# Kernel tuning notes

Hardware: AMD Instinct MI355X
Metric: run time of the kernel (lower is better)

The kernel has to match this reference:

```python
import jax, jax.numpy as jnp
import numpy as np

B, S, D, H = 4, 2048, 1024, 16
DK = D // H  # 64


def setup_inputs() -> dict:
    key = jax.random.key(0)
    ks = jax.random.split(key, 9)
    x = jax.random.normal(ks[0], (B, S, D), dtype=jnp.float32)
    # causal mask, broadcast over batch and heads
    attn_mask = jnp.tril(jnp.ones((S, S), dtype=jnp.int32))[None, None]
    scale = 0.02
    Wq = jax.random.normal(ks[1], (D, D), dtype=jnp.float32) * scale
    Wk = jax.random.normal(ks[2], (D, D), dtype=jnp.float32) * scale
    Wv = jax.random.normal(ks[3], (D, D), dtype=jnp.float32) * scale
    Wo = jax.random.normal(ks[4], (D, D), dtype=jnp.float32) * scale
    bq = jax.random.normal(ks[5], (D,), dtype=jnp.float32) * scale
    bk = jax.random.normal(ks[6], (D,), dtype=jnp.float32) * scale
    bv = jax.random.normal(ks[7], (D,), dtype=jnp.float32) * scale
    bo = jax.random.normal(ks[8], (D,), dtype=jnp.float32) * scale
    return {"x": x, "attn_mask": attn_mask, "Wq": Wq, "bq": bq, "Wk": Wk,
            "bk": bk, "Wv": Wv, "bv": bv, "Wo": Wo, "bo": bo}


def reference(x, attn_mask, Wq, bq, Wk, bk, Wv, bv, Wo, bo):
    b, s, d = x.shape
    # projections -> [b, h, s, dk]
    def proj(W, bias):
        return (x @ W + bias).reshape(b, s, H, DK).transpose(0, 2, 1, 3)
    q = proj(Wq, bq)
    k = proj(Wk, bk)
    v = proj(Wv, bv)
    # scores [b, h, s, s]
    scores = jnp.einsum('bhqd,bhkd->bhqk', q, k) / jnp.sqrt(jnp.float32(DK))
    scores = jnp.where(attn_mask == 0, jnp.float32(-1e9), scores)
    probs = jax.nn.softmax(scores, axis=-1)  # dropout_rate=0 -> identity
    attn_out = jnp.einsum('bhqk,bhkd->bhqd', probs, v)
    # combine heads -> [b, s, d], then output projection
    attn_out = attn_out.transpose(0, 2, 1, 3).reshape(b, s, d)
    return attn_out @ Wo + bo
```

## Files before the change

kernel.cpp:

```cpp
#include <hip/hip_runtime.h>
#include <hip/hip_bf16.h>
#include <stdint.h>

#define S_LEN 2048
#define DMODEL 1024
#define NH 16
#define DK 64
#define BATCH 4
#define KDIM 1024
#define SCQ 0.18033688f

using bf16 = __hip_bfloat16;
using bf162 = __hip_bfloat162;

typedef __bf16 v_bf16x8 __attribute__((ext_vector_type(8)));
typedef short v_s16x4 __attribute__((ext_vector_type(4)));
typedef float v_f32x4 __attribute__((ext_vector_type(4)));

union PackB4 { v_s16x4 v; bf162 h[2]; };

__device__ __forceinline__ void gll16(const void* g, void* l) {
    __builtin_amdgcn_global_load_lds(
        (__attribute__((address_space(1))) unsigned int*)g,
        (__attribute__((address_space(3))) unsigned int*)l, 16, 0, 0);
}

struct alignas(8) BF4 { bf16 a, b, c, d; };

__global__ __launch_bounds__(256) void cvt_f32_bf16(const float* __restrict__ in,
                                                    bf16* __restrict__ out) {
    size_t i = ((size_t)blockIdx.x * 256 + threadIdx.x) * 4;
    float4 v = *(const float4*)(in + i);
    BF4 r;
    r.a = __float2bfloat16(v.x);
    r.b = __float2bfloat16(v.y);
    r.c = __float2bfloat16(v.z);
    r.d = __float2bfloat16(v.w);
    *(BF4*)(out + i) = r;
}

__global__ __launch_bounds__(256) void transpose_cvt4(
    const float* __restrict__ W0, const float* __restrict__ W1,
    const float* __restrict__ W2, const float* __restrict__ W3,
    bf16* __restrict__ Wt4) {
    __shared__ float tile[32][33];
    const int z = blockIdx.z;
    const float* W = (z == 0) ? W0 : (z == 1) ? W1 : (z == 2) ? W2 : W3;
    bf16* Wt = Wt4 + (size_t)z * DMODEL * DMODEL;
    const float sc = (z == 0) ? SCQ : 1.0f;
    int tx = threadIdx.x, ty = threadIdx.y;
    int k0 = blockIdx.x * 32, n0 = blockIdx.y * 32;
    #pragma unroll
    for (int i = 0; i < 4; i++) {
        int k = k0 + ty + 8 * i;
        tile[ty + 8 * i][tx] = W[(size_t)k * DMODEL + n0 + tx];
    }
    __syncthreads();
    #pragma unroll
    for (int i = 0; i < 4; i++) {
        int n = n0 + ty + 8 * i;
        Wt[(size_t)n * DMODEL + k0 + tx] = __float2bfloat16(tile[tx][ty + 8 * i] * sc);
    }
}

__global__ __launch_bounds__(256) void gemm_qkv(
    const bf16* __restrict__ A, const bf16* __restrict__ Wt4,
    const float* __restrict__ bq, const float* __restrict__ bk,
    const float* __restrict__ bv,
    bf16* __restrict__ Qo, bf16* __restrict__ Ko, bf16* __restrict__ Vto)
{
    __shared__ __align__(16) short As[128 * 32];
    __shared__ __align__(16) short Bs[128 * 32];
    const int z = blockIdx.z;
    const bf16* Bt = Wt4 + (size_t)z * DMODEL * DMODEL;
    const float* bias = (z == 0) ? bq : (z == 1) ? bk : bv;
    const float bsc = (z == 0) ? SCQ : 1.0f;

    const int t = threadIdx.x;
    const int lane = t & 63;
    const int wave = t >> 6;
    const int quad = lane >> 4;
    const int l15 = lane & 15;
    const int m0 = blockIdx.x * 128;
    const int n0 = blockIdx.y * 128;
    const int wRow = (wave >> 1) * 64;
    const int wCol = (wave & 1) * 64;

    const int r0 = t >> 2, p0 = t & 3;
    const int r1 = (t + 256) >> 2, p1 = (t + 256) & 3;

    const short* ArowBase = (z == 2) ? Bs : As;
    const short* BrowBase = (z == 2) ? As : Bs;

    v_f32x4 acc[4][4] = {};

    for (int k0 = 0; k0 < KDIM; k0 += 32) {
        __syncthreads();
        gll16(A  + (size_t)(m0 + r0) * KDIM + k0 + p0 * 8, As + (size_t)t * 8);
        gll16(A  + (size_t)(m0 + r1) * KDIM + k0 + p1 * 8, As + (size_t)t * 8 + 2048);
        gll16(Bt + (size_t)(n0 + r0) * KDIM + k0 + p0 * 8, Bs + (size_t)t * 8);
        gll16(Bt + (size_t)(n0 + r1) * KDIM + k0 + p1 * 8, Bs + (size_t)t * 8 + 2048);
        __syncthreads();

        v_bf16x8 af[4], bfr[4];
        #pragma unroll
        for (int mt = 0; mt < 4; mt++) {
            int r = wRow + mt * 16 + l15;
            af[mt] = *(const v_bf16x8*)(ArowBase + r * 32 + quad * 8);
        }
        #pragma unroll
        for (int nt = 0; nt < 4; nt++) {
            int r = wCol + nt * 16 + l15;
            bfr[nt] = *(const v_bf16x8*)(BrowBase + r * 32 + quad * 8);
        }
        #pragma unroll
        for (int mt = 0; mt < 4; mt++)
            #pragma unroll
            for (int nt = 0; nt < 4; nt++)
                acc[mt][nt] = __builtin_amdgcn_mfma_f32_16x16x32_bf16(
                    af[mt], bfr[nt], acc[mt][nt], 0, 0, 0);
    }

    if (z != 2) {
        bf16* C = (z == 0) ? Qo : Ko;
        float bvv[4];
        #pragma unroll
        for (int nt = 0; nt < 4; nt++)
            bvv[nt] = bias[n0 + wCol + nt * 16 + l15] * bsc;
        #pragma unroll
        for (int mt = 0; mt < 4; mt++)
            #pragma unroll
            for (int nt = 0; nt < 4; nt++)
                #pragma unroll
                for (int r = 0; r < 4; r++) {
                    int row = m0 + wRow + mt * 16 + quad * 4 + r;
                    int col = n0 + wCol + nt * 16 + l15;
                    int b = row >> 11, s = row & (S_LEN - 1);
                    int h = col >> 6, dk = col & (DK - 1);
                    C[(((size_t)(b * NH + h)) * S_LEN + s) * DK + dk] =
                        __float2bfloat16(acc[mt][nt][r] + bvv[nt]);
                }
    } else {
        float bvv[4][4];
        #pragma unroll
        for (int mt = 0; mt < 4; mt++)
            #pragma unroll
            for (int r = 0; r < 4; r++)
                bvv[mt][r] = bias[n0 + wRow + mt * 16 + quad * 4 + r];
        #pragma unroll
        for (int mt = 0; mt < 4; mt++)
            #pragma unroll
            for (int nt = 0; nt < 4; nt++)
                #pragma unroll
                for (int r = 0; r < 4; r++) {
                    int ng = n0 + wRow + mt * 16 + quad * 4 + r;
                    int rowg = m0 + wCol + nt * 16 + l15;
                    int b = rowg >> 11, s = rowg & (S_LEN - 1);
                    int h = ng >> 6, dk = ng & (DK - 1);
                    Vto[(((size_t)(b * NH + h)) * DK + dk) * S_LEN + s] =
                        __float2bfloat16(acc[mt][nt][r] + bvv[mt][r]);
                }
    }
}

__global__ __launch_bounds__(256) void gemm_o(
    const bf16* __restrict__ A, const bf16* __restrict__ Bt,
    const float* __restrict__ bias, float* __restrict__ C)
{
    __shared__ __align__(16) short As[128 * 32];
    __shared__ __align__(16) short Bs[128 * 32];
    const int t = threadIdx.x;
    const int lane = t & 63;
    const int wave = t >> 6;
    const int quad = lane >> 4;
    const int l15 = lane & 15;
    const int m0 = blockIdx.x * 128;
    const int n0 = blockIdx.y * 128;
    const int wRow = (wave >> 1) * 64;
    const int wCol = (wave & 1) * 64;

    const int r0 = t >> 2, p0 = t & 3;
    const int r1 = (t + 256) >> 2, p1 = (t + 256) & 3;

    v_f32x4 acc[4][4] = {};

    for (int k0 = 0; k0 < KDIM; k0 += 32) {
        __syncthreads();
        gll16(A  + (size_t)(m0 + r0) * KDIM + k0 + p0 * 8, As + (size_t)t * 8);
        gll16(A  + (size_t)(m0 + r1) * KDIM + k0 + p1 * 8, As + (size_t)t * 8 + 2048);
        gll16(Bt + (size_t)(n0 + r0) * KDIM + k0 + p0 * 8, Bs + (size_t)t * 8);
        gll16(Bt + (size_t)(n0 + r1) * KDIM + k0 + p1 * 8, Bs + (size_t)t * 8 + 2048);
        __syncthreads();

        v_bf16x8 af[4], bfr[4];
        #pragma unroll
        for (int mt = 0; mt < 4; mt++) {
            int r = wRow + mt * 16 + l15;
            af[mt] = *(const v_bf16x8*)(As + r * 32 + quad * 8);
        }
        #pragma unroll
        for (int nt = 0; nt < 4; nt++) {
            int r = wCol + nt * 16 + l15;
            bfr[nt] = *(const v_bf16x8*)(Bs + r * 32 + quad * 8);
        }
        #pragma unroll
        for (int mt = 0; mt < 4; mt++)
            #pragma unroll
            for (int nt = 0; nt < 4; nt++)
                acc[mt][nt] = __builtin_amdgcn_mfma_f32_16x16x32_bf16(
                    af[mt], bfr[nt], acc[mt][nt], 0, 0, 0);
    }

    float bvv[4];
    #pragma unroll
    for (int nt = 0; nt < 4; nt++) bvv[nt] = bias[n0 + wCol + nt * 16 + l15];

    #pragma unroll
    for (int mt = 0; mt < 4; mt++)
        #pragma unroll
        for (int nt = 0; nt < 4; nt++)
            #pragma unroll
            for (int r = 0; r < 4; r++) {
                int row = m0 + wRow + mt * 16 + quad * 4 + r;
                int col = n0 + wCol + nt * 16 + l15;
                C[(size_t)row * DMODEL + col] = acc[mt][nt][r] + bvv[nt];
            }
}

__global__ __launch_bounds__(256) void attn_mfma(
    const bf16* __restrict__ Qg, const bf16* __restrict__ Kg,
    const bf16* __restrict__ Vtg, bf16* __restrict__ Og)
{
    __shared__ __align__(16) short lds[16384];

    const int t = threadIdx.x;
    const int lane = t & 63;
    const int wave = t >> 6;
    const int quad = lane >> 4;
    const int l15 = lane & 15;
    const int bh = blockIdx.x;
    const int ybal[16] = {15, 8, 7, 0, 14, 9, 6, 1, 13, 10, 5, 2, 12, 11, 4, 3};
    const int by = blockIdx.y;
    const int yy = ybal[(by & 3) * 4 + (by >> 2)];
    const int q0 = yy * 128;
    const int ntiles = 2 * (yy + 1);

    const size_t baseK = (size_t)bh * S_LEN * DK;
    const size_t baseVt = (size_t)bh * DK * S_LEN;

    const int cr = t >> 3;
    const int cs = (t & 7) ^ (cr & 7);
    const bf16* srcK = Kg + baseK + (size_t)cr * DK + cs * 8;
    const bf16* srcV = Vtg + baseVt + (size_t)cr * S_LEN + cs * 8;

    v_bf16x8 qf[2][2];
    #pragma unroll
    for (int qt = 0; qt < 2; qt++) {
        int q = q0 + wave * 32 + qt * 16 + l15;
        #pragma unroll
        for (int kc = 0; kc < 2; kc++)
            qf[qt][kc] = *(const v_bf16x8*)(Qg + baseK + (size_t)q * DK + kc * 32 + quad * 8);
    }

    v_f32x4 oacc[2][4] = {};
    float lrun[2] = {0.f, 0.f};

    {
        short* Kd = lds;
        short* Vd = lds + 4096;
        gll16(srcK, Kd + t * 8);
        gll16(srcK + 32 * DK, Kd + t * 8 + 2048);
        gll16(srcV, Vd + t * 8);
        gll16(srcV + 32 * S_LEN, Vd + t * 8 + 2048);
    }
    __syncthreads();

    int cur = 0;
    for (int tt = 0; tt < ntiles; tt++) {
        if (tt + 1 < ntiles) {
            short* Kd = lds + (cur ^ 1) * 8192;
            short* Vd = Kd + 4096;
            const bf16* sk = srcK + (size_t)(tt + 1) * (64 * DK);
            const bf16* sv = srcV + (size_t)(tt + 1) * 64;
            gll16(sk, Kd + t * 8);
            gll16(sk + 32 * DK, Kd + t * 8 + 2048);
            gll16(sv, Vd + t * 8);
            gll16(sv + 32 * S_LEN, Vd + t * 8 + 2048);
        }
        const short* Ks = lds + cur * 8192;
        const short* Vs = Ks + 4096;

        v_f32x4 s_[4][2];
        __builtin_amdgcn_s_setprio(1);
        #pragma unroll
        for (int kt = 0; kt < 4; kt++) {
            int krow = kt * 16 + l15;
            v_bf16x8 kf0 = *(const v_bf16x8*)(Ks + krow * 64 + ((quad) ^ (krow & 7)) * 8);
            v_bf16x8 kf1 = *(const v_bf16x8*)(Ks + krow * 64 + ((4 + quad) ^ (krow & 7)) * 8);
            #pragma unroll
            for (int qt = 0; qt < 2; qt++) {
                v_f32x4 a = {};
                a = __builtin_amdgcn_mfma_f32_16x16x32_bf16(kf0, qf[qt][0], a, 0, 0, 0);
                a = __builtin_amdgcn_mfma_f32_16x16x32_bf16(kf1, qf[qt][1], a, 0, 0, 0);
                s_[kt][qt] = a;
            }
        }
        __builtin_amdgcn_s_setprio(0);

        if (tt >= ntiles - 2) {
            int kbase = (tt - (ntiles - 2)) * 64;
            #pragma unroll
            for (int kt = 0; kt < 4; kt++)
                #pragma unroll
                for (int qt = 0; qt < 2; qt++) {
                    int qq = wave * 32 + qt * 16 + l15;
                    #pragma unroll
                    for (int r = 0; r < 4; r++) {
                        int key = kbase + kt * 16 + quad * 4 + r;
                        if (key > qq) s_[kt][qt][r] = -1e30f;
                    }
                }
        }

        #pragma unroll
        for (int kt = 0; kt < 4; kt++)
            #pragma unroll
            for (int qt = 0; qt < 2; qt++) {
                float p0 = __builtin_amdgcn_exp2f(s_[kt][qt][0]);
                float p1 = __builtin_amdgcn_exp2f(s_[kt][qt][1]);
                float p2 = __builtin_amdgcn_exp2f(s_[kt][qt][2]);
                float p3 = __builtin_amdgcn_exp2f(s_[kt][qt][3]);
                s_[kt][qt][0] = p0; s_[kt][qt][1] = p1;
                s_[kt][qt][2] = p2; s_[kt][qt][3] = p3;
                lrun[qt] += (p0 + p1) + (p2 + p3);
            }

        __builtin_amdgcn_s_setprio(1);
        #pragma unroll
        for (int kt = 0; kt < 4; kt++) {
            v_s16x4 vf[4];
            #pragma unroll
            for (int dt = 0; dt < 4; dt++) {
                vf[dt] = *(const v_s16x4*)(Vs + (dt * 16 + l15) * 64 +
                                           ((kt * 2 + (quad >> 1)) ^ (l15 & 7)) * 8 +
                                           (quad & 1) * 4);
            }
            #pragma unroll
            for (int qt = 0; qt < 2; qt++) {
                PackB4 pu;
                pu.h[0] = __float22bfloat162_rn(make_float2(s_[kt][qt][0], s_[kt][qt][1]));
                pu.h[1] = __float22bfloat162_rn(make_float2(s_[kt][qt][2], s_[kt][qt][3]));
                #pragma unroll
                for (int dt = 0; dt < 4; dt++)
                    oacc[qt][dt] = __builtin_amdgcn_mfma_f32_16x16x16bf16_1k(
                        vf[dt], pu.v, oacc[qt][dt], 0, 0, 0);
            }
        }
        __builtin_amdgcn_s_setprio(0);

        __syncthreads();
        cur ^= 1;
    }

    #pragma unroll
    for (int qt = 0; qt < 2; qt++) {
        lrun[qt] += __shfl_xor(lrun[qt], 16);
        lrun[qt] += __shfl_xor(lrun[qt], 32);
    }
    #pragma unroll
    for (int qt = 0; qt < 2; qt++) {
        float inv = 1.f / lrun[qt];
        int qloc = wave * 32 + qt * 16 + l15;
        #pragma unroll
        for (int dt = 0; dt < 4; dt++) {
            PackB4 ou;
            ou.h[0] = __float22bfloat162_rn(
                make_float2(oacc[qt][dt][0] * inv, oacc[qt][dt][1] * inv));
            ou.h[1] = __float22bfloat162_rn(
                make_float2(oacc[qt][dt][2] * inv, oacc[qt][dt][3] * inv));
            *(v_s16x4*)(lds + qloc * 72 + dt * 16 + quad * 4) = ou.v;
        }
    }
    __syncthreads();
    {
        const int b = bh >> 4, h = bh & 15;
        int row = t >> 1, half = t & 1;
        size_t gbase = (((size_t)b * S_LEN + q0 + row) * NH + h) * DK + half * 32;
        #pragma unroll
        for (int j = 0; j < 4; j++)
            *(uint4*)(Og + gbase + j * 8) =
                *(const uint4*)(lds + row * 72 + half * 32 + j * 8);
    }
}

extern "C" void kernel_launch(void* const* d_in, const int* in_sizes, int n_in,
                              void* d_out, int out_size, void* d_ws, size_t ws_size,
                              hipStream_t stream) {
    const float* x  = (const float*)d_in[0];
    const float* Wq = (const float*)d_in[2];
    const float* bq = (const float*)d_in[3];
    const float* Wk = (const float*)d_in[4];
    const float* bk = (const float*)d_in[5];
    const float* Wv = (const float*)d_in[6];
    const float* bv = (const float*)d_in[7];
    const float* Wo = (const float*)d_in[8];
    const float* bo = (const float*)d_in[9];
    float* out = (float*)d_out;

    const size_t TEN = (size_t)BATCH * S_LEN * DMODEL * sizeof(bf16);
    char* ws = (char*)d_ws;
    bf16* xb  = (bf16*)ws;
    bf16* Vt  = (bf16*)(ws + TEN);
    bf16* Wt4 = (bf16*)(ws + 2 * TEN);
    bf16* Q   = (bf16*)d_out;
    bf16* Kt  = (bf16*)((char*)d_out + TEN);
    bf16* AO  = xb;

    hipLaunchKernelGGL(cvt_f32_bf16, dim3(BATCH * S_LEN * DMODEL / 1024), dim3(256),
                       0, stream, x, xb);

    hipLaunchKernelGGL(transpose_cvt4, dim3(DMODEL / 32, DMODEL / 32, 4), dim3(32, 8),
                       0, stream, Wq, Wk, Wv, Wo, Wt4);

    hipLaunchKernelGGL(gemm_qkv, dim3(BATCH * S_LEN / 128, DMODEL / 128, 3), dim3(256),
                       0, stream, xb, Wt4, bq, bk, bv, Q, Kt, Vt);

    hipLaunchKernelGGL(attn_mfma, dim3(BATCH * NH, S_LEN / 128), dim3(256),
                       0, stream, Q, Kt, Vt, AO);

    hipLaunchKernelGGL(gemm_o, dim3(BATCH * S_LEN / 128, DMODEL / 128), dim3(256),
                       0, stream, AO, Wt4 + (size_t)3 * DMODEL * DMODEL, bo, out);
}
```

Measured before the change: 272.2 us.

## Double-buffer GEMM LDS tiles and merge prep kernels into one launch

Both projection GEMMs now use a double-buffered LDS ring: the next K-tile's global-to-LDS loads are issued before the MFMA work on the current tile, with one barrier per iteration instead of two. MFMA sections are wrapped in s_setprio to favor math issue. The x conversion and weight transpose kernels are merged into a single prep launch, using a fifth z-slice for the x cast. LDS use per block doubles, which may reduce occupancy.

Result: faster. 255.6 us (median of 2 runs) (-6.1%).

```diff
diff --git a/kernel.cpp b/kernel.cpp
--- a/kernel.cpp
+++ b/kernel.cpp
@@ -27,28 +27,35 @@
 
 struct alignas(8) BF4 { bf16 a, b, c, d; };
 
-__global__ __launch_bounds__(256) void cvt_f32_bf16(const float* __restrict__ in,
-                                                    bf16* __restrict__ out) {
-    size_t i = ((size_t)blockIdx.x * 256 + threadIdx.x) * 4;
-    float4 v = *(const float4*)(in + i);
-    BF4 r;
-    r.a = __float2bfloat16(v.x);
-    r.b = __float2bfloat16(v.y);
-    r.c = __float2bfloat16(v.z);
-    r.d = __float2bfloat16(v.w);
-    *(BF4*)(out + i) = r;
-}
-
-__global__ __launch_bounds__(256) void transpose_cvt4(
+__global__ __launch_bounds__(256) void prep(
+    const float* __restrict__ x, bf16* __restrict__ xb,
     const float* __restrict__ W0, const float* __restrict__ W1,
     const float* __restrict__ W2, const float* __restrict__ W3,
-    bf16* __restrict__ Wt4) {
+    bf16* __restrict__ Wt4)
+{
+    const int z = blockIdx.z;
+    const int t = threadIdx.x;
+    if (z == 4) {
+        int bid = blockIdx.y * 32 + blockIdx.x;
+        size_t base4 = (size_t)bid * 2048 + t;
+        #pragma unroll
+        for (int j = 0; j < 8; j++) {
+            size_t i4 = base4 + j * 256;
+            float4 v = *(const float4*)(x + i4 * 4);
+            BF4 r;
+            r.a = __float2bfloat16(v.x);
+            r.b = __float2bfloat16(v.y);
+            r.c = __float2bfloat16(v.z);
+            r.d = __float2bfloat16(v.w);
+            *(BF4*)(xb + i4 * 4) = r;
+        }
+        return;
+    }
     __shared__ float tile[32][33];
-    const int z = blockIdx.z;
     const float* W = (z == 0) ? W0 : (z == 1) ? W1 : (z == 2) ? W2 : W3;
     bf16* Wt = Wt4 + (size_t)z * DMODEL * DMODEL;
     const float sc = (z == 0) ? SCQ : 1.0f;
-    int tx = threadIdx.x, ty = threadIdx.y;
+    int tx = t & 31, ty = t >> 5;
     int k0 = blockIdx.x * 32, n0 = blockIdx.y * 32;
     #pragma unroll
     for (int i = 0; i < 4; i++) {
@@ -69,8 +76,7 @@
     const float* __restrict__ bv,
     bf16* __restrict__ Qo, bf16* __restrict__ Ko, bf16* __restrict__ Vto)
 {
-    __shared__ __align__(16) short As[128 * 32];
-    __shared__ __align__(16) short Bs[128 * 32];
+    __shared__ __align__(16) short lds[16384];
     const int z = blockIdx.z;
     const bf16* Bt = Wt4 + (size_t)z * DMODEL * DMODEL;
     const float* bias = (z == 0) ? bq : (z == 1) ? bk : bv;
@@ -89,18 +95,33 @@
     const int r0 = t >> 2, p0 = t & 3;
     const int r1 = (t + 256) >> 2, p1 = (t + 256) & 3;
 
-    const short* ArowBase = (z == 2) ? Bs : As;
-    const short* BrowBase = (z == 2) ? As : Bs;
+    const bf16* gA0 = A  + (size_t)(m0 + r0) * KDIM + p0 * 8;
+    const bf16* gA1 = A  + (size_t)(m0 + r1) * KDIM + p1 * 8;
+    const bf16* gB0 = Bt + (size_t)(n0 + r0) * KDIM + p0 * 8;
+    const bf16* gB1 = Bt + (size_t)(n0 + r1) * KDIM + p1 * 8;
 
     v_f32x4 acc[4][4] = {};
 
+    gll16(gA0, lds + t * 8);
+    gll16(gA1, lds + t * 8 + 2048);
+    gll16(gB0, lds + 4096 + t * 8);
+    gll16(gB1, lds + 4096 + t * 8 + 2048);
+    __syncthreads();
+
+    int cur = 0;
     for (int k0 = 0; k0 < KDIM; k0 += 32) {
-        __syncthreads();
-        gll16(A  + (size_t)(m0 + r0) * KDIM + k0 + p0 * 8, As + (size_t)t * 8);
-        gll16(A  + (size_t)(m0 + r1) * KDIM + k0 + p1 * 8, As + (size_t)t * 8 + 2048);
-        gll16(Bt + (size_t)(n0 + r0) * KDIM + k0 + p0 * 8, Bs + (size_t)t * 8);
-        gll16(Bt + (size_t)(n0 + r1) * KDIM + k0 + p1 * 8, Bs + (size_t)t * 8 + 2048);
-        __syncthreads();
+        if (k0 + 32 < KDIM) {
+            short* Ad = lds + (cur ^ 1) * 8192;
+            short* Bd = Ad + 4096;
+            gll16(gA0 + k0 + 32, Ad + t * 8);
+            gll16(gA1 + k0 + 32, Ad + t * 8 + 2048);
+            gll16(gB0 + k0 + 32, Bd + t * 8);
+            gll16(gB1 + k0 + 32, Bd + t * 8 + 2048);
+        }
+        const short* As = lds + cur * 8192;
+        const short* Bs = As + 4096;
+        const short* ArowBase = (z == 2) ? Bs : As;
+        const short* BrowBase = (z == 2) ? As : Bs;
 
         v_bf16x8 af[4], bfr[4];
         #pragma unroll
@@ -113,12 +134,17 @@
             int r = wCol + nt * 16 + l15;
             bfr[nt] = *(const v_bf16x8*)(BrowBase + r * 32 + quad * 8);
         }
+        __builtin_amdgcn_s_setprio(1);
         #pragma unroll
         for (int mt = 0; mt < 4; mt++)
             #pragma unroll
             for (int nt = 0; nt < 4; nt++)
                 acc[mt][nt] = __builtin_amdgcn_mfma_f32_16x16x32_bf16(
                     af[mt], bfr[nt], acc[mt][nt], 0, 0, 0);
+        __builtin_amdgcn_s_setprio(0);
+
+        __syncthreads();
+        cur ^= 1;
     }
 
     if (z != 2) {
@@ -167,8 +193,7 @@
     const bf16* __restrict__ A, const bf16* __restrict__ Bt,
     const float* __restrict__ bias, float* __restrict__ C)
 {
-    __shared__ __align__(16) short As[128 * 32];
-    __shared__ __align__(16) short Bs[128 * 32];
+    __shared__ __align__(16) short lds[16384];
     const int t = threadIdx.x;
     const int lane = t & 63;
     const int wave = t >> 6;
@@ -182,15 +207,31 @@
     const int r0 = t >> 2, p0 = t & 3;
     const int r1 = (t + 256) >> 2, p1 = (t + 256) & 3;
 
+    const bf16* gA0 = A  + (size_t)(m0 + r0) * KDIM + p0 * 8;
+    const bf16* gA1 = A  + (size_t)(m0 + r1) * KDIM + p1 * 8;
+    const bf16* gB0 = Bt + (size_t)(n0 + r0) * KDIM + p0 * 8;
+    const bf16* gB1 = Bt + (size_t)(n0 + r1) * KDIM + p1 * 8;
+
     v_f32x4 acc[4][4] = {};
 
+    gll16(gA0, lds + t * 8);
+    gll16(gA1, lds + t * 8 + 2048);
+    gll16(gB0, lds + 4096 + t * 8);
+    gll16(gB1, lds + 4096 + t * 8 + 2048);
+    __syncthreads();
+
+    int cur = 0;
     for (int k0 = 0; k0 < KDIM; k0 += 32) {
-        __syncthreads();
-        gll16(A  + (size_t)(m0 + r0) * KDIM + k0 + p0 * 8, As + (size_t)t * 8);
-        gll16(A  + (size_t)(m0 + r1) * KDIM + k0 + p1 * 8, As + (size_t)t * 8 + 2048);
-        gll16(Bt + (size_t)(n0 + r0) * KDIM + k0 + p0 * 8, Bs + (size_t)t * 8);
-        gll16(Bt + (size_t)(n0 + r1) * KDIM + k0 + p1 * 8, Bs + (size_t)t * 8 + 2048);
-        __syncthreads();
+        if (k0 + 32 < KDIM) {
+            short* Ad = lds + (cur ^ 1) * 8192;
+            short* Bd = Ad + 4096;
+            gll16(gA0 + k0 + 32, Ad + t * 8);
+            gll16(gA1 + k0 + 32, Ad + t * 8 + 2048);
+            gll16(gB0 + k0 + 32, Bd + t * 8);
+            gll16(gB1 + k0 + 32, Bd + t * 8 + 2048);
+        }
+        const short* As = lds + cur * 8192;
+        const short* Bs = As + 4096;
 
         v_bf16x8 af[4], bfr[4];
         #pragma unroll
@@ -203,12 +244,17 @@
             int r = wCol + nt * 16 + l15;
             bfr[nt] = *(const v_bf16x8*)(Bs + r * 32 + quad * 8);
         }
+        __builtin_amdgcn_s_setprio(1);
         #pragma unroll
         for (int mt = 0; mt < 4; mt++)
             #pragma unroll
             for (int nt = 0; nt < 4; nt++)
                 acc[mt][nt] = __builtin_amdgcn_mfma_f32_16x16x32_bf16(
                     af[mt], bfr[nt], acc[mt][nt], 0, 0, 0);
+        __builtin_amdgcn_s_setprio(0);
+
+        __syncthreads();
+        cur ^= 1;
     }
 
     float bvv[4];
@@ -416,11 +462,8 @@
     bf16* Kt  = (bf16*)((char*)d_out + TEN);
     bf16* AO  = xb;
 
-    hipLaunchKernelGGL(cvt_f32_bf16, dim3(BATCH * S_LEN * DMODEL / 1024), dim3(256),
-                       0, stream, x, xb);
-
-    hipLaunchKernelGGL(transpose_cvt4, dim3(DMODEL / 32, DMODEL / 32, 4), dim3(32, 8),
-                       0, stream, Wq, Wk, Wv, Wo, Wt4);
+    hipLaunchKernelGGL(prep, dim3(32, 32, 5), dim3(256),
+                       0, stream, x, xb, Wq, Wk, Wv, Wo, Wt4);
 
     hipLaunchKernelGGL(gemm_qkv, dim3(BATCH * S_LEN / 128, DMODEL / 128, 3), dim3(256),
                        0, stream, xb, Wt4, bq, bk, bv, Q, Kt, Vt);
```
